# Kernel optimization log

Hardware: AMD Instinct MI355X
Metric: run time of the kernel (lower is better)

## Reference

```python
import jax, jax.numpy as jnp
import numpy as np

N, E, D = 10000, 160000, 512


def setup_inputs() -> dict:
    key = jax.random.key(0)
    ks = jax.random.split(key, 5)
    x = jax.random.normal(ks[0], (N, D), dtype=jnp.float32)
    edge_index = jax.random.randint(ks[1], (2, E), 0, N, dtype=jnp.int32)
    W = jax.random.normal(ks[2], (D, D), dtype=jnp.float32) * (1.0 / np.sqrt(D))
    a_src = jax.random.normal(ks[3], (D,), dtype=jnp.float32) * 0.1
    a_dst = jax.random.normal(ks[4], (D,), dtype=jnp.float32) * 0.1
    bias = jnp.zeros((D,), dtype=jnp.float32)
    return {"x": x, "edge_index": edge_index, "W": W,
            "a_src": a_src, "a_dst": a_dst, "bias": bias}


def reference(x, edge_index, W, a_src, a_dst, bias):
    n = x.shape[0]
    # PyG GATConv default: add self-loops
    loops = jnp.arange(n, dtype=edge_index.dtype)
    src = jnp.concatenate([edge_index[0], loops])  # [E+N]
    dst = jnp.concatenate([edge_index[1], loops])  # [E+N]

    h = x @ W.T                                    # [N, D] linear projection
    e_src = h @ a_src                              # [N]
    e_dst = h @ a_dst                              # [N]
    e = e_src[src] + e_dst[dst]                    # [E+N]
    neg_slope = 0.2
    e = jnp.where(e > 0, e, neg_slope * e)         # leaky_relu

    # per-destination softmax (stable); self-loops guarantee non-empty segments
    m = jax.ops.segment_max(e, dst, num_segments=n)
    e = jnp.exp(e - m[dst])
    s = jax.ops.segment_sum(e, dst, num_segments=n)
    alpha = e / s[dst]                             # [E+N]

    msg = alpha[:, None] * h[src]                  # [E+N, D]
    out = jax.ops.segment_sum(msg, dst, num_segments=n) + bias  # [N, D]

    # module forward: x + elu(gat(x, edge_index))
    return x + jax.nn.elu(out)
```

## Files before the change

### kernel.cpp

```cpp
#include <hip/hip_runtime.h>
#include <hip/hip_bf16.h>

using bf16x8 = __attribute__((ext_vector_type(8))) __bf16;
using f32x4  = __attribute__((ext_vector_type(4))) float;
typedef unsigned int u32;

#define DFEAT 512
#define SLOTS 64
#define FS 128
#define NSLICE 4

static __device__ __forceinline__ unsigned short f2bfbits(float f) {
    union { float f; unsigned int u; } v; v.f = f;
    unsigned int u = v.u;
    unsigned int r = (u + 0x7fffu + ((u >> 16) & 1u)) >> 16;
    return (unsigned short)r;
}

static __device__ __forceinline__ void gload16(const unsigned short* g, unsigned short* l) {
    __builtin_amdgcn_global_load_lds(
        (const __attribute__((address_space(1))) u32*)g,
        (__attribute__((address_space(3))) u32*)l, 16, 0, 0);
}

__global__ __launch_bounds__(256) void cvt_scatter_kernel(
    const float* __restrict__ x, const float* __restrict__ w,
    unsigned short* __restrict__ Xb, unsigned short* __restrict__ Wb,
    const int* __restrict__ srcv, const int* __restrict__ dstv,
    int* __restrict__ cur, int* __restrict__ slot,
    int nx4, int ntot4, int E, int T)
{
    int i = blockIdx.x * 256 + threadIdx.x;
    if (i < ntot4) {
        const float* in = (i < nx4) ? x : w;
        unsigned short* o = (i < nx4) ? Xb : Wb;
        int j = (i < nx4) ? i : i - nx4;
        float4 v = ((const float4*)in)[j];
        ushort4 u;
        u.x = f2bfbits(v.x); u.y = f2bfbits(v.y);
        u.z = f2bfbits(v.z); u.w = f2bfbits(v.w);
        ((ushort4*)o)[j] = u;
    }
    if (i < T) {
        int s, d;
        if (i < E) { s = srcv[i]; d = dstv[i]; }
        else       { s = d = i - E; }
        int pos = atomicAdd(&cur[d], 1);
        if (pos < SLOTS) slot[(size_t)d * SLOTS + pos] = s;
    }
}

__global__ __launch_bounds__(256, 3) void gemm_h_kernel(
    const unsigned short* __restrict__ X, const unsigned short* __restrict__ Wm,
    const float* __restrict__ avs, const float* __restrict__ avd,
    unsigned short* __restrict__ H, float* __restrict__ es, float* __restrict__ ed,
    int N)
{
    __shared__ __align__(16) unsigned short Asm[2][128 * 64];
    __shared__ __align__(16) unsigned short Bsm[2][64 * 64];

    int L = blockIdx.x;
    int xcd = L & 7;
    int q   = L >> 3;
    int rpan = (q >> 3) * 8 + xcd;
    int cpan = q & 7;
    int rowPanels = (N + 127) >> 7;
    if (rpan >= rowPanels) return;
    int bm = rpan * 128;
    int bn = cpan * 64;

    int tid  = threadIdx.x;
    int wave = tid >> 6;
    int lane = tid & 63;
    int l15  = lane & 15;
    int quad = lane >> 4;

    int srow   = lane >> 3;
    int schunk = (lane & 7) ^ srow;
    const unsigned short* gA0;
    const unsigned short* gA1;
    const unsigned short* gA2;
    const unsigned short* gA3;
    {
        int r0 = bm + wave * 32 +  0 + srow; r0 = r0 < N ? r0 : N - 1;
        int r1 = bm + wave * 32 +  8 + srow; r1 = r1 < N ? r1 : N - 1;
        int r2 = bm + wave * 32 + 16 + srow; r2 = r2 < N ? r2 : N - 1;
        int r3 = bm + wave * 32 + 24 + srow; r3 = r3 < N ? r3 : N - 1;
        gA0 = X + (size_t)r0 * DFEAT + schunk * 8;
        gA1 = X + (size_t)r1 * DFEAT + schunk * 8;
        gA2 = X + (size_t)r2 * DFEAT + schunk * 8;
        gA3 = X + (size_t)r3 * DFEAT + schunk * 8;
    }
    const unsigned short* gB0 = Wm + (size_t)(bn + wave * 16 + srow) * DFEAT + schunk * 8;
    const unsigned short* gB1 = gB0 + (size_t)8 * DFEAT;

    auto stage = [&](int buf, int s) {
        int ko = s * 64;
        gload16(gA0 + ko, &Asm[buf][(wave * 32 +  0) * 64]);
        gload16(gA1 + ko, &Asm[buf][(wave * 32 +  8) * 64]);
        gload16(gA2 + ko, &Asm[buf][(wave * 32 + 16) * 64]);
        gload16(gA3 + ko, &Asm[buf][(wave * 32 + 24) * 64]);
        gload16(gB0 + ko, &Bsm[buf][(wave * 16 + 0) * 64]);
        gload16(gB1 + ko, &Bsm[buf][(wave * 16 + 8) * 64]);
    };

    f32x4 acc[2][4] = {};
    int xa = l15 & 7;
    int aoff0 = (wave * 32 +  0 + l15) * 128;
    int aoff1 = (wave * 32 + 16 + l15) * 128;

    auto compute = [&](int buf) {
        const char* Ab = (const char*)&Asm[buf][0];
        const char* Bb = (const char*)&Bsm[buf][0];
        #pragma unroll
        for (int ks = 0; ks < 2; ++ks) {
            int cb = ((ks * 4 + quad) ^ xa) * 16;
            bf16x8 a0 = *(const bf16x8*)(Ab + aoff0 + cb);
            bf16x8 a1 = *(const bf16x8*)(Ab + aoff1 + cb);
            bf16x8 b0 = *(const bf16x8*)(Bb + (0 * 16 + l15) * 128 + cb);
            bf16x8 b1 = *(const bf16x8*)(Bb + (1 * 16 + l15) * 128 + cb);
            bf16x8 b2 = *(const bf16x8*)(Bb + (2 * 16 + l15) * 128 + cb);
            bf16x8 b3 = *(const bf16x8*)(Bb + (3 * 16 + l15) * 128 + cb);
            acc[0][0] = __builtin_amdgcn_mfma_f32_16x16x32_bf16(a0, b0, acc[0][0], 0, 0, 0);
            acc[1][0] = __builtin_amdgcn_mfma_f32_16x16x32_bf16(a1, b0, acc[1][0], 0, 0, 0);
            acc[0][1] = __builtin_amdgcn_mfma_f32_16x16x32_bf16(a0, b1, acc[0][1], 0, 0, 0);
            acc[1][1] = __builtin_amdgcn_mfma_f32_16x16x32_bf16(a1, b1, acc[1][1], 0, 0, 0);
            acc[0][2] = __builtin_amdgcn_mfma_f32_16x16x32_bf16(a0, b2, acc[0][2], 0, 0, 0);
            acc[1][2] = __builtin_amdgcn_mfma_f32_16x16x32_bf16(a1, b2, acc[1][2], 0, 0, 0);
            acc[0][3] = __builtin_amdgcn_mfma_f32_16x16x32_bf16(a0, b3, acc[0][3], 0, 0, 0);
            acc[1][3] = __builtin_amdgcn_mfma_f32_16x16x32_bf16(a1, b3, acc[1][3], 0, 0, 0);
        }
    };

    stage(0, 0);
    __syncthreads();
    int buf = 0;
    for (int s = 0; s < 7; ++s) {
        stage(buf ^ 1, s + 1);
        compute(buf);
        __syncthreads();
        buf ^= 1;
    }
    compute(buf);

    float as[4], ad[4];
    #pragma unroll
    for (int nt = 0; nt < 4; ++nt) {
        as[nt] = avs[bn + nt * 16 + l15];
        ad[nt] = avd[bn + nt * 16 + l15];
    }

    #pragma unroll
    for (int mt = 0; mt < 2; ++mt) {
        int rbase = bm + wave * 32 + mt * 16 + quad * 4;
        #pragma unroll
        for (int nt = 0; nt < 4; ++nt) {
            int col = bn + nt * 16 + l15;
            #pragma unroll
            for (int r = 0; r < 4; ++r) {
                int row = rbase + r;
                if (row < N) H[(size_t)row * DFEAT + col] = f2bfbits(acc[mt][nt][r]);
            }
        }
        #pragma unroll
        for (int r = 0; r < 4; ++r) {
            float ps = acc[mt][0][r] * as[0] + acc[mt][1][r] * as[1]
                     + acc[mt][2][r] * as[2] + acc[mt][3][r] * as[3];
            float pd = acc[mt][0][r] * ad[0] + acc[mt][1][r] * ad[1]
                     + acc[mt][2][r] * ad[2] + acc[mt][3][r] * ad[3];
            #pragma unroll
            for (int m = 1; m < 16; m <<= 1) {
                ps += __shfl_xor(ps, m);
                pd += __shfl_xor(pd, m);
            }
            int row = rbase + r;
            if (l15 == 0 && row < N) {
                atomicAdd(&es[row], ps);
                atomicAdd(&ed[row], pd);
            }
        }
    }
}

__global__ __launch_bounds__(256) void aggregate_kernel(
    const unsigned short* __restrict__ H, const float* __restrict__ x,
    const float* __restrict__ bias,
    const int* __restrict__ cur, const int* __restrict__ slot,
    const float* __restrict__ es, const float* __restrict__ ed,
    float* __restrict__ out, int N)
{
    int gw   = blockIdx.x * 4 + (threadIdx.x >> 6);
    int lane = threadIdx.x & 63;
    if (gw >= NSLICE * N) return;
    int slice = 0, node = gw;
    if (node >= 2 * N) { slice = 2; node -= 2 * N; }
    if (node >= N)     { slice += 1; node -= N; }

    int k = cur[node];
    if (k > SLOTS) k = SLOTS;

    int   s = 0;
    float w = 0.f;
    if (lane < k) {
        s = slot[(size_t)node * SLOTS + lane];
        float e = es[s] + ed[node];
        e = e > 0.f ? e : 0.2f * e;
        w = __expf(e);
    }
    float denom = w;
    #pragma unroll
    for (int off = 32; off > 0; off >>= 1) denom += __shfl_xor(denom, off);
    float inv = 1.0f / denom;

    float a0 = 0.f, a1 = 0.f;
    const char* Hb = (const char*)H + slice * (FS * 2) + lane * 4;

    auto fma2 = [&](u32 hv, float wj) {
        a0 += wj * __uint_as_float(hv << 16);
        a1 += wj * __uint_as_float(hv & 0xffff0000u);
    };

    int j = 0;
    for (; j + 7 < k; j += 8) {
        int   s0 = __shfl(s, j),     s1 = __shfl(s, j + 1);
        int   s2 = __shfl(s, j + 2), s3 = __shfl(s, j + 3);
        int   s4 = __shfl(s, j + 4), s5 = __shfl(s, j + 5);
        int   s6 = __shfl(s, j + 6), s7 = __shfl(s, j + 7);
        float w0 = __shfl(w, j),     w1 = __shfl(w, j + 1);
        float w2 = __shfl(w, j + 2), w3 = __shfl(w, j + 3);
        float w4 = __shfl(w, j + 4), w5 = __shfl(w, j + 5);
        float w6 = __shfl(w, j + 6), w7 = __shfl(w, j + 7);
        u32 h0 = *(const u32*)(Hb + (size_t)s0 * 1024);
        u32 h1 = *(const u32*)(Hb + (size_t)s1 * 1024);
        u32 h2 = *(const u32*)(Hb + (size_t)s2 * 1024);
        u32 h3 = *(const u32*)(Hb + (size_t)s3 * 1024);
        u32 h4 = *(const u32*)(Hb + (size_t)s4 * 1024);
        u32 h5 = *(const u32*)(Hb + (size_t)s5 * 1024);
        u32 h6 = *(const u32*)(Hb + (size_t)s6 * 1024);
        u32 h7 = *(const u32*)(Hb + (size_t)s7 * 1024);
        fma2(h0, w0); fma2(h1, w1); fma2(h2, w2); fma2(h3, w3);
        fma2(h4, w4); fma2(h5, w5); fma2(h6, w6); fma2(h7, w7);
    }
    if (j + 3 < k) {
        int   s0 = __shfl(s, j),     s1 = __shfl(s, j + 1);
        int   s2 = __shfl(s, j + 2), s3 = __shfl(s, j + 3);
        float w0 = __shfl(w, j),     w1 = __shfl(w, j + 1);
        float w2 = __shfl(w, j + 2), w3 = __shfl(w, j + 3);
        u32 h0 = *(const u32*)(Hb + (size_t)s0 * 1024);
        u32 h1 = *(const u32*)(Hb + (size_t)s1 * 1024);
        u32 h2 = *(const u32*)(Hb + (size_t)s2 * 1024);
        u32 h3 = *(const u32*)(Hb + (size_t)s3 * 1024);
        fma2(h0, w0); fma2(h1, w1); fma2(h2, w2); fma2(h3, w3);
        j += 4;
    }
    for (; j < k; ++j) {
        u32 hv = *(const u32*)(Hb + (size_t)__shfl(s, j) * 1024);
        fma2(hv, __shfl(w, j));
    }

    int c = slice * FS + lane * 2;
    float2 bv = *(const float2*)(bias + c);
    float2 xv = *(const float2*)(x + (size_t)node * DFEAT + c);
    float r0 = a0 * inv + bv.x;
    float r1 = a1 * inv + bv.y;
    r0 = r0 > 0.f ? r0 : __expf(r0) - 1.f;
    r1 = r1 > 0.f ? r1 : __expf(r1) - 1.f;
    float2 o = make_float2(xv.x + r0, xv.y + r1);
    *(float2*)(out + (size_t)node * DFEAT + c) = o;
}

extern "C" void kernel_launch(void* const* d_in, const int* in_sizes, int n_in,
                              void* d_out, int out_size, void* d_ws, size_t ws_size,
                              hipStream_t stream)
{
    const float* x    = (const float*)d_in[0];
    const int*   edge = (const int*)d_in[1];
    const float* Wm   = (const float*)d_in[2];
    const float* avs  = (const float*)d_in[3];
    const float* avd  = (const float*)d_in[4];
    const float* bias = (const float*)d_in[5];

    const int D = DFEAT;
    const int N = in_sizes[0] / D;
    const int E = in_sizes[1] / 2;
    const int T = E + N;
    const int* srcv = edge;
    const int* dstv = edge + E;

    char* ws = (char*)d_ws;
    size_t off = 0;
    auto alloc = [&](size_t bytes) -> char* {
        char* p = ws + off;
        off += (bytes + 255) & ~(size_t)255;
        return p;
    };
    int*   cur  = (int*)alloc((size_t)N * 3 * 4);
    float* es   = (float*)(cur + N);
    float* ed   = es + N;
    int*   slot = (int*)alloc((size_t)N * SLOTS * 4);
    unsigned short* Xb = (unsigned short*)alloc((size_t)N * D * 2);
    unsigned short* Wb = (unsigned short*)alloc((size_t)D * D * 2);
    unsigned short* H  = (unsigned short*)alloc((size_t)N * D * 2);

    hipMemsetAsync(cur, 0, (size_t)N * 3 * 4, stream);

    int nx4   = (N * D) / 4;
    int ntot4 = nx4 + (D * D) / 4;
    int grid0 = (ntot4 > T ? ntot4 : T);
    cvt_scatter_kernel<<<dim3((grid0 + 255) / 256), 256, 0, stream>>>(
        x, Wm, Xb, Wb, srcv, dstv, cur, slot, nx4, ntot4, E, T);

    int rowPanels  = (N + 127) / 128;
    int rowPanels8 = ((rowPanels + 7) / 8) * 8;
    gemm_h_kernel<<<dim3(rowPanels8 * 8), 256, 0, stream>>>(
        Xb, Wb, avs, avd, H, es, ed, N);

    int aggWaves = NSLICE * N;
    aggregate_kernel<<<dim3((aggWaves * 64 + 255) / 256), 256, 0, stream>>>(
        H, x, bias, cur, slot, es, ed, (float*)d_out, N);
}
```

Baseline: 132.7 us.

## Aggregate X before projection and fuse gather with GEMM epilogue

The linear projection and the attention aggregation are reordered. Attention logits are now computed as x·(Wᵀa), using vectors vs and vd precomputed from W. The fused kernel gathers and softmax-weights the bf16 rows of X into shared memory, then multiplies by W with MFMA and applies bias, ELU and the residual in the epilogue. This removes the separate H write/read and the aggregate kernel. In exchange, each 32-node block restages all of W and performs the irregular gather inside the GEMM pipeline, at one block per CU with a large LDS footprint.

Measured after the change: 177.0 us. 1.33x slower.

```diff
diff --git a/kernel.cpp b/kernel.cpp
--- a/kernel.cpp
+++ b/kernel.cpp
@@ -7,8 +7,8 @@
 
 #define DFEAT 512
 #define SLOTS 64
-#define FS 128
-#define NSLICE 4
+#define BM 32
+#define BK 64
 
 static __device__ __forceinline__ unsigned short f2bfbits(float f) {
     union { float f; unsigned int u; } v; v.f = f;
@@ -23,104 +23,219 @@
         (__attribute__((address_space(3))) u32*)l, 16, 0, 0);
 }
 
-__global__ __launch_bounds__(256) void cvt_scatter_kernel(
-    const float* __restrict__ x, const float* __restrict__ w,
-    unsigned short* __restrict__ Xb, unsigned short* __restrict__ Wb,
+__global__ __launch_bounds__(256) void prep_kernel(
+    const float* __restrict__ Wm, const float* __restrict__ a_src,
+    const float* __restrict__ a_dst,
+    unsigned short* __restrict__ Wb, float* __restrict__ vs, float* __restrict__ vd,
     const int* __restrict__ srcv, const int* __restrict__ dstv,
-    int* __restrict__ cur, int* __restrict__ slot,
-    int nx4, int ntot4, int E, int T)
+    int* __restrict__ cur, int* __restrict__ slot, int E, int T)
 {
-    int i = blockIdx.x * 256 + threadIdx.x;
-    if (i < ntot4) {
-        const float* in = (i < nx4) ? x : w;
-        unsigned short* o = (i < nx4) ? Xb : Wb;
-        int j = (i < nx4) ? i : i - nx4;
-        float4 v = ((const float4*)in)[j];
-        ushort4 u;
-        u.x = f2bfbits(v.x); u.y = f2bfbits(v.y);
-        u.z = f2bfbits(v.z); u.w = f2bfbits(v.w);
-        ((ushort4*)o)[j] = u;
-    }
-    if (i < T) {
-        int s, d;
-        if (i < E) { s = srcv[i]; d = dstv[i]; }
-        else       { s = d = i - E; }
-        int pos = atomicAdd(&cur[d], 1);
-        if (pos < SLOTS) slot[(size_t)d * SLOTS + pos] = s;
-    }
-}
-
-__global__ __launch_bounds__(256, 3) void gemm_h_kernel(
-    const unsigned short* __restrict__ X, const unsigned short* __restrict__ Wm,
-    const float* __restrict__ avs, const float* __restrict__ avd,
-    unsigned short* __restrict__ H, float* __restrict__ es, float* __restrict__ ed,
+    int b = blockIdx.x;
+    int t = threadIdx.x;
+    if (b < 32) {
+        float s0 = 0.f, s1 = 0.f, d0 = 0.f, d1 = 0.f;
+        #pragma unroll 4
+        for (int r = 0; r < 16; ++r) {
+            int j = b * 16 + r;
+            float aj_s = a_src[j], aj_d = a_dst[j];
+            float w0 = Wm[(size_t)j * DFEAT + t];
+            float w1 = Wm[(size_t)j * DFEAT + t + 256];
+            Wb[(size_t)j * DFEAT + t]       = f2bfbits(w0);
+            Wb[(size_t)j * DFEAT + t + 256] = f2bfbits(w1);
+            s0 += w0 * aj_s; s1 += w1 * aj_s;
+            d0 += w0 * aj_d; d1 += w1 * aj_d;
+        }
+        atomicAdd(&vs[t], s0); atomicAdd(&vs[t + 256], s1);
+        atomicAdd(&vd[t], d0); atomicAdd(&vd[t + 256], d1);
+    } else {
+        int base = (b - 32) * 1024 + t;
+        #pragma unroll
+        for (int it = 0; it < 4; ++it) {
+            int i = base + it * 256;
+            if (i < T) {
+                int s, d;
+                if (i < E) { s = srcv[i]; d = dstv[i]; }
+                else       { s = d = i - E; }
+                int pos = atomicAdd(&cur[d], 1);
+                if (pos < SLOTS) slot[(size_t)d * SLOTS + pos] = s;
+            }
+        }
+    }
+}
+
+__global__ __launch_bounds__(256) void cvt_x_kernel(
+    const float* __restrict__ x, const float* __restrict__ vs,
+    const float* __restrict__ vd,
+    unsigned short* __restrict__ Xb, float* __restrict__ es, float* __restrict__ ed,
     int N)
 {
-    __shared__ __align__(16) unsigned short Asm[2][128 * 64];
-    __shared__ __align__(16) unsigned short Bsm[2][64 * 64];
-
-    int L = blockIdx.x;
-    int xcd = L & 7;
-    int q   = L >> 3;
-    int rpan = (q >> 3) * 8 + xcd;
-    int cpan = q & 7;
-    int rowPanels = (N + 127) >> 7;
-    if (rpan >= rowPanels) return;
-    int bm = rpan * 128;
-    int bn = cpan * 64;
+    int node = (blockIdx.x * 256 + threadIdx.x) >> 6;
+    int lane = threadIdx.x & 63;
+    if (node >= N) return;
+    const float* xr = x + (size_t)node * DFEAT + lane * 8;
+    float4 v0 = *(const float4*)xr;
+    float4 v1 = *(const float4*)(xr + 4);
+    ushort4 u0, u1;
+    u0.x = f2bfbits(v0.x); u0.y = f2bfbits(v0.y);
+    u0.z = f2bfbits(v0.z); u0.w = f2bfbits(v0.w);
+    u1.x = f2bfbits(v1.x); u1.y = f2bfbits(v1.y);
+    u1.z = f2bfbits(v1.z); u1.w = f2bfbits(v1.w);
+    *(ushort4*)(Xb + (size_t)node * DFEAT + lane * 8)     = u0;
+    *(ushort4*)(Xb + (size_t)node * DFEAT + lane * 8 + 4) = u1;
+    float4 s0 = *(const float4*)(vs + lane * 8);
+    float4 s1 = *(const float4*)(vs + lane * 8 + 4);
+    float4 d0 = *(const float4*)(vd + lane * 8);
+    float4 d1 = *(const float4*)(vd + lane * 8 + 4);
+    float ps = v0.x*s0.x + v0.y*s0.y + v0.z*s0.z + v0.w*s0.w
+             + v1.x*s1.x + v1.y*s1.y + v1.z*s1.z + v1.w*s1.w;
+    float pd = v0.x*d0.x + v0.y*d0.y + v0.z*d0.z + v0.w*d0.w
+             + v1.x*d1.x + v1.y*d1.y + v1.z*d1.z + v1.w*d1.w;
+    #pragma unroll
+    for (int m = 1; m < 64; m <<= 1) {
+        ps += __shfl_xor(ps, m);
+        pd += __shfl_xor(pd, m);
+    }
+    if (lane == 0) { es[node] = ps; ed[node] = pd; }
+}
+
+__global__ __launch_bounds__(512, 1) void gat_fused_kernel(
+    const unsigned short* __restrict__ Xb, const unsigned short* __restrict__ Wb,
+    const float* __restrict__ x, const float* __restrict__ bias,
+    const int* __restrict__ cur, const int* __restrict__ slot,
+    const float* __restrict__ es, const float* __restrict__ ed,
+    float* __restrict__ out, int N)
+{
+    __shared__ __align__(16) unsigned short Bsm[2][512 * 64];
+    __shared__ __align__(16) unsigned short Asm[2][BM * 64];
+    __shared__ int   srcS[BM][SLOTS];
+    __shared__ float wS[BM][SLOTS + 1];
+    __shared__ float invS[BM];
+    __shared__ int   kcntS[BM];
 
     int tid  = threadIdx.x;
     int wave = tid >> 6;
     int lane = tid & 63;
     int l15  = lane & 15;
     int quad = lane >> 4;
-
-    int srow   = lane >> 3;
-    int schunk = (lane & 7) ^ srow;
-    const unsigned short* gA0;
-    const unsigned short* gA1;
-    const unsigned short* gA2;
-    const unsigned short* gA3;
-    {
-        int r0 = bm + wave * 32 +  0 + srow; r0 = r0 < N ? r0 : N - 1;
-        int r1 = bm + wave * 32 +  8 + srow; r1 = r1 < N ? r1 : N - 1;
-        int r2 = bm + wave * 32 + 16 + srow; r2 = r2 < N ? r2 : N - 1;
-        int r3 = bm + wave * 32 + 24 + srow; r3 = r3 < N ? r3 : N - 1;
-        gA0 = X + (size_t)r0 * DFEAT + schunk * 8;
-        gA1 = X + (size_t)r1 * DFEAT + schunk * 8;
-        gA2 = X + (size_t)r2 * DFEAT + schunk * 8;
-        gA3 = X + (size_t)r3 * DFEAT + schunk * 8;
-    }
-    const unsigned short* gB0 = Wm + (size_t)(bn + wave * 16 + srow) * DFEAT + schunk * 8;
-    const unsigned short* gB1 = gB0 + (size_t)8 * DFEAT;
-
-    auto stage = [&](int buf, int s) {
-        int ko = s * 64;
-        gload16(gA0 + ko, &Asm[buf][(wave * 32 +  0) * 64]);
-        gload16(gA1 + ko, &Asm[buf][(wave * 32 +  8) * 64]);
-        gload16(gA2 + ko, &Asm[buf][(wave * 32 + 16) * 64]);
-        gload16(gA3 + ko, &Asm[buf][(wave * 32 + 24) * 64]);
-        gload16(gB0 + ko, &Bsm[buf][(wave * 16 + 0) * 64]);
-        gload16(gB1 + ko, &Bsm[buf][(wave * 16 + 8) * 64]);
+    int n0   = blockIdx.x * BM;
+
+    if (tid < BM) {
+        int node = n0 + tid;
+        int k = (node < N) ? cur[node] : 0;
+        kcntS[tid] = k > SLOTS ? SLOTS : k;
+    }
+    __syncthreads();
+
+    for (int idx = tid; idx < BM * SLOTS; idx += 512) {
+        int nn = idx >> 6, j = idx & 63;
+        float w = 0.f; int s = 0;
+        if (j < kcntS[nn]) {
+            int node = n0 + nn;
+            s = slot[(size_t)node * SLOTS + j];
+            float e = es[s] + ed[node];
+            e = e > 0.f ? e : 0.2f * e;
+            w = __expf(e);
+        }
+        srcS[nn][j] = s;
+        wS[nn][j] = w;
+    }
+
+    int brl    = lane >> 3;
+    int bchunk = (lane & 7) ^ brl;
+    auto stageB = [&](int buf, int s) {
+        int ko = s * BK;
+        #pragma unroll
+        for (int p = 0; p < 8; ++p) {
+            int n = wave * 8 + p * 64 + brl;
+            gload16(Wb + (size_t)n * DFEAT + ko + bchunk * 8,
+                    &Bsm[buf][(size_t)(wave * 8 + p * 64) * 64]);
+        }
+    };
+    stageB(0, 0);
+    __syncthreads();
+
+    if (tid < BM) {
+        float d = 0.f;
+        int k = kcntS[tid];
+        for (int j = 0; j < k; ++j) d += wS[tid][j];
+        invS[tid] = (k > 0) ? 1.0f / d : 0.f;
+    }
+    __syncthreads();
+
+    int gn   = tid >> 4;
+    int gsub = tid & 15;
+    int goff = gsub * 8;
+    int adst = gn * 128 + (((gsub >> 1) ^ (gn & 7)) * 16) + (gsub & 1) * 8;
+    const char* Xc = (const char*)Xb;
+
+    auto gatherA = [&](int buf, int s) {
+        int ko2 = s * BK * 2;
+        int kc = kcntS[gn];
+        float a0 = 0.f, a1 = 0.f, a2 = 0.f, a3 = 0.f;
+        auto fma4 = [&](uint2 h, float w) {
+            a0 += w * __uint_as_float(h.x << 16);
+            a1 += w * __uint_as_float(h.x & 0xffff0000u);
+            a2 += w * __uint_as_float(h.y << 16);
+            a3 += w * __uint_as_float(h.y & 0xffff0000u);
+        };
+        int j = 0;
+        for (; j + 7 < kc; j += 8) {
+            int   q0 = srcS[gn][j],   q1 = srcS[gn][j+1];
+            int   q2 = srcS[gn][j+2], q3 = srcS[gn][j+3];
+            int   q4 = srcS[gn][j+4], q5 = srcS[gn][j+5];
+            int   q6 = srcS[gn][j+6], q7 = srcS[gn][j+7];
+            float w0 = wS[gn][j],   w1 = wS[gn][j+1];
+            float w2 = wS[gn][j+2], w3 = wS[gn][j+3];
+            float w4 = wS[gn][j+4], w5 = wS[gn][j+5];
+            float w6 = wS[gn][j+6], w7 = wS[gn][j+7];
+            uint2 h0 = *(const uint2*)(Xc + (size_t)q0 * 1024 + ko2 + goff);
+            uint2 h1 = *(const uint2*)(Xc + (size_t)q1 * 1024 + ko2 + goff);
+            uint2 h2 = *(const uint2*)(Xc + (size_t)q2 * 1024 + ko2 + goff);
+            uint2 h3 = *(const uint2*)(Xc + (size_t)q3 * 1024 + ko2 + goff);
+            uint2 h4 = *(const uint2*)(Xc + (size_t)q4 * 1024 + ko2 + goff);
+            uint2 h5 = *(const uint2*)(Xc + (size_t)q5 * 1024 + ko2 + goff);
+            uint2 h6 = *(const uint2*)(Xc + (size_t)q6 * 1024 + ko2 + goff);
+            uint2 h7 = *(const uint2*)(Xc + (size_t)q7 * 1024 + ko2 + goff);
+            fma4(h0, w0); fma4(h1, w1); fma4(h2, w2); fma4(h3, w3);
+            fma4(h4, w4); fma4(h5, w5); fma4(h6, w6); fma4(h7, w7);
+        }
+        if (j + 3 < kc) {
+            int   q0 = srcS[gn][j],   q1 = srcS[gn][j+1];
+            int   q2 = srcS[gn][j+2], q3 = srcS[gn][j+3];
+            float w0 = wS[gn][j],   w1 = wS[gn][j+1];
+            float w2 = wS[gn][j+2], w3 = wS[gn][j+3];
+            uint2 h0 = *(const uint2*)(Xc + (size_t)q0 * 1024 + ko2 + goff);
+            uint2 h1 = *(const uint2*)(Xc + (size_t)q1 * 1024 + ko2 + goff);
+            uint2 h2 = *(const uint2*)(Xc + (size_t)q2 * 1024 + ko2 + goff);
+            uint2 h3 = *(const uint2*)(Xc + (size_t)q3 * 1024 + ko2 + goff);
+            fma4(h0, w0); fma4(h1, w1); fma4(h2, w2); fma4(h3, w3);
+            j += 4;
+        }
+        for (; j < kc; ++j) {
+            uint2 hv = *(const uint2*)(Xc + (size_t)srcS[gn][j] * 1024 + ko2 + goff);
+            fma4(hv, wS[gn][j]);
+        }
+        float inv = invS[gn];
+        ushort4 o;
+        o.x = f2bfbits(a0 * inv); o.y = f2bfbits(a1 * inv);
+        o.z = f2bfbits(a2 * inv); o.w = f2bfbits(a3 * inv);
+        *(ushort4*)((char*)&Asm[buf][0] + adst) = o;
     };
 
     f32x4 acc[2][4] = {};
     int xa = l15 & 7;
-    int aoff0 = (wave * 32 +  0 + l15) * 128;
-    int aoff1 = (wave * 32 + 16 + l15) * 128;
-
     auto compute = [&](int buf) {
         const char* Ab = (const char*)&Asm[buf][0];
         const char* Bb = (const char*)&Bsm[buf][0];
         #pragma unroll
         for (int ks = 0; ks < 2; ++ks) {
             int cb = ((ks * 4 + quad) ^ xa) * 16;
-            bf16x8 a0 = *(const bf16x8*)(Ab + aoff0 + cb);
-            bf16x8 a1 = *(const bf16x8*)(Ab + aoff1 + cb);
-            bf16x8 b0 = *(const bf16x8*)(Bb + (0 * 16 + l15) * 128 + cb);
-            bf16x8 b1 = *(const bf16x8*)(Bb + (1 * 16 + l15) * 128 + cb);
-            bf16x8 b2 = *(const bf16x8*)(Bb + (2 * 16 + l15) * 128 + cb);
-            bf16x8 b3 = *(const bf16x8*)(Bb + (3 * 16 + l15) * 128 + cb);
+            bf16x8 a0 = *(const bf16x8*)(Ab + (0 * 16 + l15) * 128 + cb);
+            bf16x8 a1 = *(const bf16x8*)(Ab + (1 * 16 + l15) * 128 + cb);
+            bf16x8 b0 = *(const bf16x8*)(Bb + (size_t)(wave * 64 +  0 + l15) * 128 + cb);
+            bf16x8 b1 = *(const bf16x8*)(Bb + (size_t)(wave * 64 + 16 + l15) * 128 + cb);
+            bf16x8 b2 = *(const bf16x8*)(Bb + (size_t)(wave * 64 + 32 + l15) * 128 + cb);
+            bf16x8 b3 = *(const bf16x8*)(Bb + (size_t)(wave * 64 + 48 + l15) * 128 + cb);
             acc[0][0] = __builtin_amdgcn_mfma_f32_16x16x32_bf16(a0, b0, acc[0][0], 0, 0, 0);
             acc[1][0] = __builtin_amdgcn_mfma_f32_16x16x32_bf16(a1, b0, acc[1][0], 0, 0, 0);
             acc[0][1] = __builtin_amdgcn_mfma_f32_16x16x32_bf16(a0, b1, acc[0][1], 0, 0, 0);
@@ -132,141 +247,37 @@
         }
     };
 
-    stage(0, 0);
+    gatherA(0, 0);
     __syncthreads();
     int buf = 0;
     for (int s = 0; s < 7; ++s) {
-        stage(buf ^ 1, s + 1);
+        stageB(buf ^ 1, s + 1);
+        gatherA(buf ^ 1, s + 1);
         compute(buf);
         __syncthreads();
         buf ^= 1;
     }
     compute(buf);
 
-    float as[4], ad[4];
+    float bcol[4];
     #pragma unroll
-    for (int nt = 0; nt < 4; ++nt) {
-        as[nt] = avs[bn + nt * 16 + l15];
-        ad[nt] = avd[bn + nt * 16 + l15];
-    }
-
+    for (int nt = 0; nt < 4; ++nt) bcol[nt] = bias[wave * 64 + nt * 16 + l15];
     #pragma unroll
     for (int mt = 0; mt < 2; ++mt) {
-        int rbase = bm + wave * 32 + mt * 16 + quad * 4;
-        #pragma unroll
-        for (int nt = 0; nt < 4; ++nt) {
-            int col = bn + nt * 16 + l15;
-            #pragma unroll
-            for (int r = 0; r < 4; ++r) {
-                int row = rbase + r;
-                if (row < N) H[(size_t)row * DFEAT + col] = f2bfbits(acc[mt][nt][r]);
-            }
-        }
         #pragma unroll
         for (int r = 0; r < 4; ++r) {
-            float ps = acc[mt][0][r] * as[0] + acc[mt][1][r] * as[1]
-                     + acc[mt][2][r] * as[2] + acc[mt][3][r] * as[3];
-            float pd = acc[mt][0][r] * ad[0] + acc[mt][1][r] * ad[1]
-                     + acc[mt][2][r] * ad[2] + acc[mt][3][r] * ad[3];
-            #pragma unroll
-            for (int m = 1; m < 16; m <<= 1) {
-                ps += __shfl_xor(ps, m);
-                pd += __shfl_xor(pd, m);
+            int node = n0 + mt * 16 + quad * 4 + r;
+            if (node < N) {
+                #pragma unroll
+                for (int nt = 0; nt < 4; ++nt) {
+                    int col = wave * 64 + nt * 16 + l15;
+                    float v = acc[mt][nt][r] + bcol[nt];
+                    v = v > 0.f ? v : __expf(v) - 1.f;
+                    out[(size_t)node * DFEAT + col] = x[(size_t)node * DFEAT + col] + v;
+                }
             }
-            int row = rbase + r;
-            if (l15 == 0 && row < N) {
-                atomicAdd(&es[row], ps);
-                atomicAdd(&ed[row], pd);
-            }
-        }
-    }
-}
-
-__global__ __launch_bounds__(256) void aggregate_kernel(
-    const unsigned short* __restrict__ H, const float* __restrict__ x,
-    const float* __restrict__ bias,
-    const int* __restrict__ cur, const int* __restrict__ slot,
-    const float* __restrict__ es, const float* __restrict__ ed,
-    float* __restrict__ out, int N)
-{
-    int gw   = blockIdx.x * 4 + (threadIdx.x >> 6);
-    int lane = threadIdx.x & 63;
-    if (gw >= NSLICE * N) return;
-    int slice = 0, node = gw;
-    if (node >= 2 * N) { slice = 2; node -= 2 * N; }
-    if (node >= N)     { slice += 1; node -= N; }
-
-    int k = cur[node];
-    if (k > SLOTS) k = SLOTS;
-
-    int   s = 0;
-    float w = 0.f;
-    if (lane < k) {
-        s = slot[(size_t)node * SLOTS + lane];
-        float e = es[s] + ed[node];
-        e = e > 0.f ? e : 0.2f * e;
-        w = __expf(e);
-    }
-    float denom = w;
-    #pragma unroll
-    for (int off = 32; off > 0; off >>= 1) denom += __shfl_xor(denom, off);
-    float inv = 1.0f / denom;
-
-    float a0 = 0.f, a1 = 0.f;
-    const char* Hb = (const char*)H + slice * (FS * 2) + lane * 4;
-
-    auto fma2 = [&](u32 hv, float wj) {
-        a0 += wj * __uint_as_float(hv << 16);
-        a1 += wj * __uint_as_float(hv & 0xffff0000u);
-    };
-
-    int j = 0;
-    for (; j + 7 < k; j += 8) {
-        int   s0 = __shfl(s, j),     s1 = __shfl(s, j + 1);
-        int   s2 = __shfl(s, j + 2), s3 = __shfl(s, j + 3);
-        int   s4 = __shfl(s, j + 4), s5 = __shfl(s, j + 5);
-        int   s6 = __shfl(s, j + 6), s7 = __shfl(s, j + 7);
-        float w0 = __shfl(w, j),     w1 = __shfl(w, j + 1);
-        float w2 = __shfl(w, j + 2), w3 = __shfl(w, j + 3);
-        float w4 = __shfl(w, j + 4), w5 = __shfl(w, j + 5);
-        float w6 = __shfl(w, j + 6), w7 = __shfl(w, j + 7);
-        u32 h0 = *(const u32*)(Hb + (size_t)s0 * 1024);
-        u32 h1 = *(const u32*)(Hb + (size_t)s1 * 1024);
-        u32 h2 = *(const u32*)(Hb + (size_t)s2 * 1024);
-        u32 h3 = *(const u32*)(Hb + (size_t)s3 * 1024);
-        u32 h4 = *(const u32*)(Hb + (size_t)s4 * 1024);
-        u32 h5 = *(const u32*)(Hb + (size_t)s5 * 1024);
-        u32 h6 = *(const u32*)(Hb + (size_t)s6 * 1024);
-        u32 h7 = *(const u32*)(Hb + (size_t)s7 * 1024);
-        fma2(h0, w0); fma2(h1, w1); fma2(h2, w2); fma2(h3, w3);
-        fma2(h4, w4); fma2(h5, w5); fma2(h6, w6); fma2(h7, w7);
-    }
-    if (j + 3 < k) {
-        int   s0 = __shfl(s, j),     s1 = __shfl(s, j + 1);
-        int   s2 = __shfl(s, j + 2), s3 = __shfl(s, j + 3);
-        float w0 = __shfl(w, j),     w1 = __shfl(w, j + 1);
-        float w2 = __shfl(w, j + 2), w3 = __shfl(w, j + 3);
-        u32 h0 = *(const u32*)(Hb + (size_t)s0 * 1024);
-        u32 h1 = *(const u32*)(Hb + (size_t)s1 * 1024);
-        u32 h2 = *(const u32*)(Hb + (size_t)s2 * 1024);
-        u32 h3 = *(const u32*)(Hb + (size_t)s3 * 1024);
-        fma2(h0, w0); fma2(h1, w1); fma2(h2, w2); fma2(h3, w3);
-        j += 4;
-    }
-    for (; j < k; ++j) {
-        u32 hv = *(const u32*)(Hb + (size_t)__shfl(s, j) * 1024);
-        fma2(hv, __shfl(w, j));
-    }
-
-    int c = slice * FS + lane * 2;
-    float2 bv = *(const float2*)(bias + c);
-    float2 xv = *(const float2*)(x + (size_t)node * DFEAT + c);
-    float r0 = a0 * inv + bv.x;
-    float r1 = a1 * inv + bv.y;
-    r0 = r0 > 0.f ? r0 : __expf(r0) - 1.f;
-    r1 = r1 > 0.f ? r1 : __expf(r1) - 1.f;
-    float2 o = make_float2(xv.x + r0, xv.y + r1);
-    *(float2*)(out + (size_t)node * DFEAT + c) = o;
+        }
+    }
 }
 
 extern "C" void kernel_launch(void* const* d_in, const int* in_sizes, int n_in,
@@ -294,28 +305,28 @@
         off += (bytes + 255) & ~(size_t)255;
         return p;
     };
-    int*   cur  = (int*)alloc((size_t)N * 3 * 4);
-    float* es   = (float*)(cur + N);
-    float* ed   = es + N;
+    size_t curBytes = (size_t)N * 4;
+    size_t vsOff    = (curBytes + 255) & ~(size_t)255;
+    char*  zbase    = alloc(vsOff + 4096);
+    int*   cur = (int*)zbase;
+    float* vs  = (float*)(zbase + vsOff);
+    float* vd  = vs + 512;
     int*   slot = (int*)alloc((size_t)N * SLOTS * 4);
     unsigned short* Xb = (unsigned short*)alloc((size_t)N * D * 2);
     unsigned short* Wb = (unsigned short*)alloc((size_t)D * D * 2);
-    unsigned short* H  = (unsigned short*)alloc((size_t)N * D * 2);
-
-    hipMemsetAsync(cur, 0, (size_t)N * 3 * 4, stream);
-
-    int nx4   = (N * D) / 4;
-    int ntot4 = nx4 + (D * D) / 4;
-    int grid0 = (ntot4 > T ? ntot4 : T);
-    cvt_scatter_kernel<<<dim3((grid0 + 255) / 256), 256, 0, stream>>>(
-        x, Wm, Xb, Wb, srcv, dstv, cur, slot, nx4, ntot4, E, T);
-
-    int rowPanels  = (N + 127) / 128;
-    int rowPanels8 = ((rowPanels + 7) / 8) * 8;
-    gemm_h_kernel<<<dim3(rowPanels8 * 8), 256, 0, stream>>>(
-        Xb, Wb, avs, avd, H, es, ed, N);
-
-    int aggWaves = NSLICE * N;
-    aggregate_kernel<<<dim3((aggWaves * 64 + 255) / 256), 256, 0, stream>>>(
-        H, x, bias, cur, slot, es, ed, (float*)d_out, N);
-}
+    float* es = (float*)alloc((size_t)N * 4);
+    float* ed = (float*)alloc((size_t)N * 4);
+
+    hipMemsetAsync(zbase, 0, vsOff + 4096, stream);
+
+    int Gscat = (T + 1023) / 1024;
+    prep_kernel<<<dim3(32 + Gscat), 256, 0, stream>>>(
+        Wm, avs, avd, Wb, vs, vd, srcv, dstv, cur, slot, E, T);
+
+    cvt_x_kernel<<<dim3((N * 64 + 255) / 256), 256, 0, stream>>>(
+        x, vs, vd, Xb, es, ed, N);
+
+    int nodeBlocks = (N + BM - 1) / BM;
+    gat_fused_kernel<<<dim3(nodeBlocks), 512, 0, stream>>>(
+        Xb, Wb, x, bias, cur, slot, es, ed, (float*)d_out, N);
+}
```
